# Kernel tuning notes

Measured on AMD Instinct MI355X. Metric: run time of the kernel, lower is better.

Reference implementation:

```python
import jax, jax.numpy as jnp
import numpy as np

K = 3           # spatial kernel size (kernel_size[1]==kernel_size[2])
STRIDE = 1
EPS_BN = 1e-5


def unfold_replicate(t, k=K, stride=STRIDE):
    """t: (b, C, H, W) -> (b, C, k*k, H//stride, W//stride).
    Replicate-padded kxk patches, row-major window order (matches F.pad(replicate)+F.unfold)."""
    b, C, H, W = t.shape
    pad = (k - 1) // 2
    tp = jnp.pad(t, ((0, 0), (0, 0), (pad, pad), (pad, pad)), mode='edge')
    patches = [tp[:, :, di:di + H:stride, dj:dj + W:stride]
               for di in range(k) for dj in range(k)]
    return jnp.stack(patches, axis=2)


def grid_sample_3d(x, grid):
    """Trilinear grid sample, zeros padding, align_corners=True.
    x: (b,c,D,H,W); grid: (b,P,3) normalized (gx,gy,gz) -> (b,c,P)."""
    b, c, D, H, W = x.shape
    ix = (grid[..., 0] + 1.0) * 0.5 * (W - 1)
    iy = (grid[..., 1] + 1.0) * 0.5 * (H - 1)
    iz = (grid[..., 2] + 1.0) * 0.5 * (D - 1)
    x0 = jnp.floor(ix); y0 = jnp.floor(iy); z0 = jnp.floor(iz)
    fx = ix - x0; fy = iy - y0; fz = iz - z0
    x0i = x0.astype(jnp.int32); y0i = y0.astype(jnp.int32); z0i = z0.astype(jnp.int32)
    x_flat = x.reshape(b, c, D * H * W)
    gather = jax.vmap(lambda xf, idx: xf[:, idx])  # (c,N),(P) -> (c,P) per batch
    out = jnp.zeros((b, c, ix.shape[1]), dtype=x.dtype)
    for dz, wz in ((0, 1.0 - fz), (1, fz)):
        zi = z0i + dz
        for dy, wy in ((0, 1.0 - fy), (1, fy)):
            yi = y0i + dy
            for dx, wx in ((0, 1.0 - fx), (1, fx)):
                xi = x0i + dx
                valid = ((zi >= 0) & (zi < D) & (yi >= 0) & (yi < H)
                         & (xi >= 0) & (xi < W))
                idx = (jnp.clip(zi, 0, D - 1) * H + jnp.clip(yi, 0, H - 1)) * W \
                      + jnp.clip(xi, 0, W - 1)
                w = (wz * wy * wx) * valid.astype(x.dtype)
                out = out + w[:, None, :] * gather(x_flat, idx)
    return out


def gca_cost(x, dp, normal, intri):
    b, c, d, H, W = x.shape
    k2 = K * K
    h, w = H // STRIDE, W // STRIDE
    ctr = k2 // 2

    dp_unf = unfold_replicate(dp)        # (b, d, k2, h, w)
    n_unf = unfold_replicate(normal)     # (b, 3, k2, h, w)
    nx, ny, nz = n_unf[:, 0], n_unf[:, 1], n_unf[:, 2]

    fx = intri[:, 0, 0][:, None, None]; fy = intri[:, 1, 1][:, None, None]
    cx = intri[:, 0, 2][:, None, None]; cy = intri[:, 1, 2][:, None, None]
    yg, xg = jnp.meshgrid(jnp.arange(H, dtype=x.dtype),
                          jnp.arange(W, dtype=x.dtype), indexing='ij')
    posx = (xg[None] - cx) / fx          # (b, H, W) normalized camera rays
    posy = (yg[None] - cy) / fy
    pos_unf = unfold_replicate(jnp.stack([posx, posy], axis=1))  # (b,2,k2,h,w)
    pu, pv = pos_unf[:, 0], pos_unf[:, 1]
    pu_c = pu[:, ctr:ctr + 1]; pv_c = pv[:, ctr:ctr + 1]

    num = nx * pu_c + ny * pv_c + nz
    den = nx * pu + ny * pv + nz
    den = jnp.where(jnp.abs(den) < 1e-8, jnp.sign(den) * 1e-8, den)
    wgt = num / den
    wgt = jnp.where(jnp.isfinite(wgt), wgt, 1.0)   # (b, k2, h, w)

    dp_ctr = dp_unf[:, :, ctr]                      # (b, d, h, w)
    dp_prog = wgt[:, None] * dp_ctr[:, :, None]     # (b, d, k2, h, w)
    interval = dp_unf[:, 1] - dp_unf[:, 0]          # (b, k2, h, w)
    z = (dp_prog - dp_unf[:, 0][:, None]) / interval[:, None]  # (b,d,k2,h,w)

    xy = jnp.broadcast_to(jnp.stack([xg, yg], axis=0)[None], (b, 2, H, W))
    xy_unf = unfold_replicate(xy)                   # (b,2,k2,h,w)
    px = jnp.broadcast_to(xy_unf[:, 0][:, None], (b, d, k2, h, w))
    py = jnp.broadcast_to(xy_unf[:, 1][:, None], (b, d, k2, h, w))

    gx = px / ((W - 1) / 2.0) - 1.0
    gy = py / ((H - 1) / 2.0) - 1.0
    gz = z / ((d - 1) / 2.0) - 1.0
    grid = jnp.stack([gx, gy, gz], axis=-1).reshape(b, d * k2 * h * w, 3)

    samp = grid_sample_3d(x, grid)                  # (b, c, d*k2*h*w)
    samp = samp.reshape(b, c, d, k2, h, w).transpose(0, 1, 3, 2, 4, 5)
    return samp.reshape(b, c * k2, d, h, w)


def reference(x, dp, normal, intri, weight, gamma, beta):
    cost = gca_cost(x, dp, normal, intri)
    y = jax.lax.conv_general_dilated(
        cost, weight, window_strides=(1, 1, 1),
        padding=[(1, 1), (0, 0), (0, 0)],
        dimension_numbers=('NCDHW', 'OIDHW', 'NCDHW'))
    # BatchNorm3d (training-mode batch stats, biased var, eps=1e-5) + ReLU
    mean = jnp.mean(y, axis=(0, 2, 3, 4), keepdims=True)
    var = jnp.var(y, axis=(0, 2, 3, 4), keepdims=True)
    g = gamma.reshape(1, -1, 1, 1, 1)
    bta = beta.reshape(1, -1, 1, 1, 1)
    return jax.nn.relu(g * (y - mean) * jax.lax.rsqrt(var + EPS_BN) + bta)


def setup_inputs() -> dict:
    key = jax.random.key(0)
    ks = jax.random.split(key, 6)
    b, c, d, H, W = 1, 8, 32, 128, 128
    out_ch = 16
    x = jax.random.normal(ks[0], (b, c, d, H, W), dtype=jnp.float32)
    # monotone depth hypotheses per pixel (interval = dp[:,1]-dp[:,0] must be nonzero)
    planes = 425.0 + 10.0 * jnp.arange(d, dtype=jnp.float32)
    scale = 1.0 + 0.05 * jax.random.uniform(ks[1], (b, 1, H, W), dtype=jnp.float32)
    dp = planes[None, :, None, None] * scale                    # (b, d, H, W)
    # near-frontal unit normals so plane-homography weights stay well-conditioned
    nxy = 0.2 * jax.random.normal(ks[2], (b, 2, H, W), dtype=jnp.float32)
    nz = 1.0 + 0.1 * jax.random.normal(ks[3], (b, 1, H, W), dtype=jnp.float32)
    n = jnp.concatenate([nxy, nz], axis=1)
    normal = n / jnp.linalg.norm(n, axis=1, keepdims=True)
    intri = jnp.broadcast_to(
        jnp.array([[1100.0, 0.0, W / 2.0],
                   [0.0, 1100.0, H / 2.0],
                   [0.0, 0.0, 1.0]], dtype=jnp.float32), (b, 3, 3))
    weight = 0.05 * jax.random.normal(ks[4], (out_ch, c * K * K, 3, 1, 1),
                                      dtype=jnp.float32)
    gamma = jnp.ones((out_ch,), jnp.float32)
    beta = jnp.zeros((out_ch,), jnp.float32)
    return {"x": x, "dp": dp, "normal": normal, "intri": intri,
            "weight": weight, "gamma": gamma, "beta": beta}
```

## Files before the change

### kernel.cpp

```cpp
#include <hip/hip_runtime.h>
#include <math.h>

#define W_    128
#define H_    128
#define HW    16384
#define D_    32
#define C_IN  8
#define OC    16
#define NRED  524288.0f

#define SXS2  19
#define SXB2  1028
#define SXS   36
#define SXB   1948
#define TILE  2568

typedef __attribute__((ext_vector_type(8))) short bf16x8;
typedef __attribute__((ext_vector_type(4))) float f32x4;

union FragU { uint4 u; bf16x8 h; };


__device__ __forceinline__ unsigned bf16rne(float f) {
    unsigned u = __float_as_uint(f);
    return (u + 0x7fffu + ((u >> 16) & 1u)) >> 16;
}

__device__ __forceinline__ void init_ws(int t, const float* __restrict__ wsrc,
                                        float* __restrict__ ws) {
    if (t < 32) ws[t] = 0.f;
    uint4* af = reinterpret_cast<uint4*>(ws + 64);
    for (int e = t; e < 768; e += 256) {
        int lane = e & 63, pkd = e >> 6;
        int p = pkd / 3, kd = pkd - p * 3;
        int o = lane & 15, kg = lane >> 4;
        int ch = 2 * p + (kg >> 1);
        int jb = (kg & 1) * 8;
        unsigned dw[4];
#pragma unroll
        for (int r2 = 0; r2 < 4; ++r2) {
            int j0 = jb + 2 * r2, j1 = j0 + 1;
            unsigned b0 = (j0 < 9) ? bf16rne(wsrc[(o * 72 + ch * 9 + j0) * 3 + kd]) : 0u;
            unsigned b1 = (j1 < 9) ? bf16rne(wsrc[(o * 72 + ch * 9 + j1) * 3 + kd]) : 0u;
            dw[r2] = b0 | (b1 << 16);
        }
        af[e] = make_uint4(dw[0], dw[1], dw[2], dw[3]);
    }
}

__global__ __launch_bounds__(256) void k_init(const float* __restrict__ wsrc,
                                              float* __restrict__ ws) {
    init_ws((int)threadIdx.x, wsrc, ws);
}

__global__ __launch_bounds__(256) void k_transpose(const float* __restrict__ x,
                                                   unsigned* __restrict__ xtb,
                                                   const float* __restrict__ wsrc,
                                                   float* __restrict__ ws) {
    __shared__ float tile[32 * 132];
    int bid = blockIdx.x;
    int c  = bid >> 7;
    int ry = bid & 127;
    int t  = threadIdx.x;
    if (bid == 0) init_ws(t, wsrc, ws);
    const float* src = x + c * (D_ * HW) + ry * W_;
    for (int k = 0; k < 4; ++k) {
        int e  = t * 4 + k * 1024;
        int z  = e >> 7;
        int rx = e & 127;
        float4 v = *reinterpret_cast<const float4*>(src + z * HW + rx);
        *reinterpret_cast<float4*>(&tile[z * 132 + rx]) = v;
    }
    __syncthreads();
    int rx = t >> 1;
    int zh = (t & 1) * 16;
    unsigned dw[8];
#pragma unroll
    for (int i = 0; i < 8; ++i) {
        float lo = tile[(zh + 2 * i) * 132 + rx];
        float hi = tile[(zh + 2 * i + 1) * 132 + rx];
        asm("v_cvt_pk_bf16_f32 %0, %1, %2" : "=v"(dw[i]) : "v"(lo), "v"(hi));
    }
    unsigned* dst = xtb + (size_t)(c * HW + ry * W_ + rx) * 16 + (t & 1) * 8;
    reinterpret_cast<uint4*>(dst)[0] = make_uint4(dw[0], dw[1], dw[2], dw[3]);
    reinterpret_cast<uint4*>(dst)[1] = make_uint4(dw[4], dw[5], dw[6], dw[7]);
}

__global__ __launch_bounds__(512, 4) void k_main_bf(const unsigned* __restrict__ xtb,
                                                    const float* __restrict__ dp,
                                                    const float* __restrict__ nrm,
                                                    const float* __restrict__ intri,
                                                    const uint4* __restrict__ afr,
                                                    unsigned* __restrict__ ybf,
                                                    float* __restrict__ stats) {
    __shared__ unsigned s_poolU[2 * SXB2];
    __shared__ float s_B[2 * TILE];
    __shared__ float s_wgt[144], s_dp0[144], s_inv[144];
    __shared__ float s_red[64];

    int t   = threadIdx.x;
    int bid = blockIdx.x;
    int r_row = bid >> 3;
    int rx0   = (bid & 7) * 16;

    int seg = t / 144;
    int f   = t - seg * 144;
    int spx = f >> 3;
    int zq  = f & 7;
    int srow = min(max(r_row + seg - 1, 0), H_ - 1);
    int scol = min(max(rx0 - 1 + spx, 0), W_ - 1);
    const unsigned* gsrcU = xtb + (size_t)(srow * W_ + scol) * 16 + zq * 2;
    int colL = seg * 18 + spx;
    int sdst = colL * SXS2 + 1 + 2 * zq;

    uint2 sv;
    if (t < 432) sv = *reinterpret_cast<const uint2*>(gsrcU);

    if (t < 144) {
        int p = t / 9, j = t - p * 9;
        int jd = j / 3;
        int dy = jd - 1, dx = (j - jd * 3) - 1;
        int cpix = rx0 + p;
        int ry  = min(max(r_row + dy, 0), H_ - 1);
        int rxn = min(max(cpix + dx, 0), W_ - 1);
        int nb  = ry * W_ + rxn;
        float fx = intri[0], cx = intri[2], fy = intri[4], cy = intri[5];
        float nx = nrm[nb], ny = nrm[HW + nb], nz = nrm[2 * HW + nb];
        float pu  = ((float)rxn  - cx) / fx;
        float pv  = ((float)ry   - cy) / fy;
        float puc = ((float)cpix - cx) / fx;
        float pvc = ((float)r_row - cy) / fy;
        float num = nx * puc + ny * pvc + nz;
        float den = nx * pu + ny * pv + nz;
        if (fabsf(den) < 1e-8f)
            den = (den > 0.f) ? 1e-8f : ((den < 0.f) ? -1e-8f : 0.f);
        float w = num / den;
        if (!isfinite(w)) w = 1.0f;
        float d0  = dp[nb];
        float itv = dp[HW + nb] - d0;
        s_wgt[t] = w;
        s_dp0[t] = d0;
        s_inv[t] = 1.0f / itv;
    }
    if (t < 324) {
        int b  = t / 162;
        int rm = t - b * 162;
        int col = rm / 3, w3 = rm - col * 3;
        int off = col * SXS2 + ((w3 == 0) ? 0 : (16 + w3));
        s_poolU[b * SXB2 + off] = 0u;
    }
    if (t < 16) s_B[2560 + (t >> 3) * TILE + (t & 7)] = 0.f;
    __syncthreads();
    if (t < 432) {
        s_poolU[sdst]     = sv.x;
        s_poolU[sdst + 1] = sv.y;
    }

    int px = t & 15;
    int d  = t >> 4;
    float dpv = dp[d * HW + r_row * W_ + rx0 + px];

    unsigned idq[9];
    float fza[9];
#pragma unroll
    for (int j = 0; j < 9; ++j) {
        int pj = px * 9 + j;
        int jd = j / 3;
        int jx = j - jd * 3;
        float z   = (s_wgt[pj] * dpv - s_dp0[pj]) * s_inv[pj];
        float zc  = fminf(fmaxf(z, -2.0f), 34.0f);
        float z0f = floorf(zc);
        fza[j] = zc - z0f;
        int s0 = 2 + (int)z0f;
        idq[j] = (unsigned)((jd * 18 + px + jx) * SXS2 + (s0 >> 1))
               | ((unsigned)(s0 & 1) << 16);
    }
    __syncthreads();

    f32x4 acc0 = {0.f, 0.f, 0.f, 0.f};
    f32x4 acc1 = {0.f, 0.f, 0.f, 0.f};
    f32x4 acc2 = {0.f, 0.f, 0.f, 0.f};
    f32x4 acc3 = {0.f, 0.f, 0.f, 0.f};

    int lane = t & 63;
    int wid  = t >> 6;
    int wb   = wid * 4;
    int grp  = lane >> 4;
    unsigned* sBu = reinterpret_cast<unsigned*>(s_B);
    int wrow = (d * 16 + px) * 5;

    for (int c = 0; c < C_IN; ++c) {
        if (c < 7 && t < 432)
            sv = *reinterpret_cast<const uint2*>(gsrcU + (size_t)(c + 1) * (HW * 16));
        const unsigned* PU = s_poolU + (c & 1) * SXB2;
        float cj[9];
#pragma unroll
        for (int j = 0; j < 9; ++j) {
            unsigned v = idq[j];
            unsigned q = v & 0xffffu;
            unsigned p = v >> 16;
            unsigned u0 = PU[q];
            unsigned u1 = PU[q + p];
            float a = __uint_as_float(p ? (u0 & 0xffff0000u) : (u0 << 16));
            float b = __uint_as_float(p ? (u1 << 16) : (u0 & 0xffff0000u));
            cj[j] = fmaf(fza[j], b - a, a);
        }
        unsigned dwv[5];
#pragma unroll
        for (int r2 = 0; r2 < 4; ++r2) {
            asm("v_cvt_pk_bf16_f32 %0, %1, %2"
                : "=v"(dwv[r2]) : "v"(cj[2 * r2]), "v"(cj[2 * r2 + 1]));
        }
        {
            float zz = 0.f;
            asm("v_cvt_pk_bf16_f32 %0, %1, %2"
                : "=v"(dwv[4]) : "v"(cj[8]), "v"(zz));
        }
        {
            int wo = wrow + (c & 1) * TILE;
            sBu[wo + 0] = dwv[0];
            sBu[wo + 1] = dwv[1];
            sBu[wo + 2] = dwv[2];
            sBu[wo + 3] = dwv[3];
            sBu[wo + 4] = dwv[4];
        }
        if (c < 7 && t < 432) {
            int ds2 = ((c + 1) & 1) * SXB2 + sdst;
            s_poolU[ds2]     = sv.x;
            s_poolU[ds2 + 1] = sv.y;
        }
        __syncthreads();

        if (c & 1) {
            int p = c >> 1;
            FragU a0, a1, a2;
            a0.u = afr[(p * 3 + 0) * 64 + lane];
            a1.u = afr[(p * 3 + 1) * 64 + lane];
            a2.u = afr[(p * 3 + 2) * 64 + lane];
            int boff = ((grp & 1) ? 4 : 0) + ((grp >> 1) ? TILE : 0);
#pragma unroll
            for (int q = 0; q < 6; ++q) {
                int db = wb - 1 + q;
                if (db < 0 || db > 31) continue;
                FragU bf;
                int base = (db * 16 + px) * 5 + boff;
                bf.u.x = sBu[base + 0];
                bf.u.y = sBu[base + 1];
                bf.u.z = sBu[base + 2];
                bf.u.w = sBu[base + 3];
                if (q - 0 >= 0 && q - 0 < 4)
                    *(q == 0 ? &acc0 : q == 1 ? &acc1 : q == 2 ? &acc2 : &acc3) =
                        __builtin_amdgcn_mfma_f32_16x16x32_bf16(a0.h, bf.h,
                            *(q == 0 ? &acc0 : q == 1 ? &acc1 : q == 2 ? &acc2 : &acc3), 0, 0, 0);
                if (q - 1 >= 0 && q - 1 < 4)
                    *(q == 1 ? &acc0 : q == 2 ? &acc1 : q == 3 ? &acc2 : &acc3) =
                        __builtin_amdgcn_mfma_f32_16x16x32_bf16(a1.h, bf.h,
                            *(q == 1 ? &acc0 : q == 2 ? &acc1 : q == 3 ? &acc2 : &acc3), 0, 0, 0);
                if (q - 2 >= 0 && q - 2 < 4)
                    *(q == 2 ? &acc0 : q == 3 ? &acc1 : q == 4 ? &acc2 : &acc3) =
                        __builtin_amdgcn_mfma_f32_16x16x32_bf16(a2.h, bf.h,
                            *(q == 2 ? &acc0 : q == 3 ? &acc1 : q == 4 ? &acc2 : &acc3), 0, 0, 0);
            }
            __syncthreads();
        }
    }

    float* s_b = s_B;
    float bns[4], bnq[4];
    int o_l = t >> 7;
    int dd  = (t >> 2) & 31;
    int q4  = t & 3;
#pragma unroll
    for (int oo = 0; oo < 4; ++oo) {
        if (grp == oo) {
#pragma unroll
            for (int r2 = 0; r2 < 4; ++r2) {
                s_b[(r2 * 32 + wb + 0) * 17 + px] = acc0[r2];
                s_b[(r2 * 32 + wb + 1) * 17 + px] = acc1[r2];
                s_b[(r2 * 32 + wb + 2) * 17 + px] = acc2[r2];
                s_b[(r2 * 32 + wb + 3) * 17 + px] = acc3[r2];
            }
        }
        __syncthreads();
        const float* brow = &s_b[(o_l * 32 + dd) * 17 + q4 * 4];
        float4 yv;
        yv.x = brow[0]; yv.y = brow[1]; yv.z = brow[2]; yv.w = brow[3];
        int o = oo * 4 + o_l;
        size_t base = (size_t)(o * 32 + dd) * HW + r_row * W_ + rx0 + q4 * 4;
        unsigned dA, dB;
        asm("v_cvt_pk_bf16_f32 %0, %1, %2" : "=v"(dA) : "v"(yv.x), "v"(yv.y));
        asm("v_cvt_pk_bf16_f32 %0, %1, %2" : "=v"(dB) : "v"(yv.z), "v"(yv.w));
        uint2 wv; wv.x = dA; wv.y = dB;
        reinterpret_cast<uint2*>(ybf)[base >> 2] = wv;
        bns[oo] = yv.x + yv.y + yv.z + yv.w;
        bnq[oo] = yv.x * yv.x + yv.y * yv.y + yv.z * yv.z + yv.w * yv.w;
        __syncthreads();
    }

#pragma unroll
    for (int oo = 0; oo < 4; ++oo) {
        float s = bns[oo], sq = bnq[oo];
#pragma unroll
        for (int m = 1; m < 64; m <<= 1) {
            s  += __shfl_xor(s, m, 64);
            sq += __shfl_xor(sq, m, 64);
        }
        if ((t & 63) == 0) {
            int w = t >> 6;
            s_red[w * 4 + oo]      = s;
            s_red[32 + w * 4 + oo] = sq;
        }
    }
    __syncthreads();
    if (t < 32) {
        int o  = t & 15;
        int oo = o >> 2, wh = o & 3;
        if (t < 16) {
            float s = s_red[(2 * wh) * 4 + oo] + s_red[(2 * wh + 1) * 4 + oo];
            atomicAdd(&stats[o], s);
        } else {
            float sq = s_red[32 + (2 * wh) * 4 + oo] + s_red[32 + (2 * wh + 1) * 4 + oo];
            atomicAdd(&stats[16 + o], sq);
        }
    }
}

__global__ __launch_bounds__(512, 4) void k_main_raw(const float* __restrict__ x,
                                                     const float* __restrict__ dp,
                                                     const float* __restrict__ nrm,
                                                     const float* __restrict__ intri,
                                                     const uint4* __restrict__ afr,
                                                     float* __restrict__ out,
                                                     float* __restrict__ stats) {
    __shared__ float s_pool[2 * SXB];
    __shared__ float s_B[2 * TILE];
    __shared__ float s_wgt[144], s_dp0[144], s_inv[144];
    __shared__ float s_red[64];

    int t   = threadIdx.x;
    int bid = blockIdx.x;
    int r_row = bid >> 3;
    int rx0   = (bid & 7) * 16;

    int seg = t / 144;
    int f   = t - seg * 144;
    int spx = f >> 3;
    int zq  = f & 7;
    int srow = min(max(r_row + seg - 1, 0), H_ - 1);
    int scol = min(max(rx0 - 1 + spx, 0), W_ - 1);
    const float* gsrc_raw = x + (srow * W_ + scol) + (size_t)(zq * 4) * HW;
    int sdst = 4 + (seg * 18 + spx) * SXS + zq * 4;

    float4 sv;
    if (t < 432) {
        sv.x = gsrc_raw[0]; sv.y = gsrc_raw[HW];
        sv.z = gsrc_raw[2 * HW]; sv.w = gsrc_raw[3 * HW];
    }

    if (t < 144) {
        int p = t / 9, j = t - p * 9;
        int jd = j / 3;
        int dy = jd - 1, dx = (j - jd * 3) - 1;
        int cpix = rx0 + p;
        int ry  = min(max(r_row + dy, 0), H_ - 1);
        int rxn = min(max(cpix + dx, 0), W_ - 1);
        int nb  = ry * W_ + rxn;
        float fx = intri[0], cx = intri[2], fy = intri[4], cy = intri[5];
        float nx = nrm[nb], ny = nrm[HW + nb], nz = nrm[2 * HW + nb];
        float pu  = ((float)rxn  - cx) / fx;
        float pv  = ((float)ry   - cy) / fy;
        float puc = ((float)cpix - cx) / fx;
        float pvc = ((float)r_row - cy) / fy;
        float num = nx * puc + ny * pvc + nz;
        float den = nx * pu + ny * pv + nz;
        if (fabsf(den) < 1e-8f)
            den = (den > 0.f) ? 1e-8f : ((den < 0.f) ? -1e-8f : 0.f);
        float w = num / den;
        if (!isfinite(w)) w = 1.0f;
        float d0  = dp[nb];
        float itv = dp[HW + nb] - d0;
        s_wgt[t] = w;
        s_dp0[t] = d0;
        s_inv[t] = 1.0f / itv;
    }
    if (t < 440) {
        int b  = t / 220;
        int rm = t - b * 220;
        int off = (rm < 4) ? rm : (4 + ((rm - 4) >> 2) * SXS + 32 + ((rm - 4) & 3));
        s_pool[b * SXB + off] = 0.f;
    }
    if (t < 16) s_B[2560 + (t >> 3) * TILE + (t & 7)] = 0.f;
    __syncthreads();
    if (t < 432) *reinterpret_cast<float4*>(&s_pool[sdst]) = sv;

    int px = t & 15;
    int d  = t >> 4;
    float dpv = dp[d * HW + r_row * W_ + rx0 + px];

    int   idx[9];
    float fza[9];
#pragma unroll
    for (int j = 0; j < 9; ++j) {
        int pj = px * 9 + j;
        int jd = j / 3;
        int jx = j - jd * 3;
        float z   = (s_wgt[pj] * dpv - s_dp0[pj]) * s_inv[pj];
        float zc  = fminf(fmaxf(z, -2.0f), 34.0f);
        float z0f = floorf(zc);
        fza[j] = zc - z0f;
        idx[j] = (jd * 18 + px + jx) * SXS + (int)z0f;
    }
    __syncthreads();

    f32x4 acc0 = {0.f, 0.f, 0.f, 0.f};
    f32x4 acc1 = {0.f, 0.f, 0.f, 0.f};
    f32x4 acc2 = {0.f, 0.f, 0.f, 0.f};
    f32x4 acc3 = {0.f, 0.f, 0.f, 0.f};

    int lane = t & 63;
    int wid  = t >> 6;
    int wb   = wid * 4;
    int grp  = lane >> 4;
    unsigned* sBu = reinterpret_cast<unsigned*>(s_B);
    int wrow = (d * 16 + px) * 5;

    for (int c = 0; c < C_IN; ++c) {
        if (c < 7 && t < 432) {
            const float* b = gsrc_raw + (size_t)(c + 1) * (D_ * HW);
            sv.x = b[0]; sv.y = b[HW]; sv.z = b[2 * HW]; sv.w = b[3 * HW];
        }
        const float* sxp = &s_pool[(c & 1) * SXB + 4];
        float cj[9];
#pragma unroll
        for (int j = 0; j < 9; ++j) {
            float a = sxp[idx[j]];
            float b = sxp[idx[j] + 1];
            cj[j] = fmaf(fza[j], b - a, a);
        }
        unsigned dwv[5];
#pragma unroll
        for (int r2 = 0; r2 < 4; ++r2) {
            asm("v_cvt_pk_bf16_f32 %0, %1, %2"
                : "=v"(dwv[r2]) : "v"(cj[2 * r2]), "v"(cj[2 * r2 + 1]));
        }
        {
            float zz = 0.f;
            asm("v_cvt_pk_bf16_f32 %0, %1, %2"
                : "=v"(dwv[4]) : "v"(cj[8]), "v"(zz));
        }
        {
            int wo = wrow + (c & 1) * TILE;
            sBu[wo + 0] = dwv[0];
            sBu[wo + 1] = dwv[1];
            sBu[wo + 2] = dwv[2];
            sBu[wo + 3] = dwv[3];
            sBu[wo + 4] = dwv[4];
        }
        if (c < 7 && t < 432) *reinterpret_cast<float4*>(&s_pool[((c + 1) & 1) * SXB + sdst]) = sv;
        __syncthreads();

        if (c & 1) {
            int p = c >> 1;
            FragU a0, a1, a2;
            a0.u = afr[(p * 3 + 0) * 64 + lane];
            a1.u = afr[(p * 3 + 1) * 64 + lane];
            a2.u = afr[(p * 3 + 2) * 64 + lane];
            int boff = ((grp & 1) ? 4 : 0) + ((grp >> 1) ? TILE : 0);
#pragma unroll
            for (int q = 0; q < 6; ++q) {
                int db = wb - 1 + q;
                if (db < 0 || db > 31) continue;
                FragU bf;
                int base = (db * 16 + px) * 5 + boff;
                bf.u.x = sBu[base + 0];
                bf.u.y = sBu[base + 1];
                bf.u.z = sBu[base + 2];
                bf.u.w = sBu[base + 3];
                if (q - 0 >= 0 && q - 0 < 4)
                    *(q == 0 ? &acc0 : q == 1 ? &acc1 : q == 2 ? &acc2 : &acc3) =
                        __builtin_amdgcn_mfma_f32_16x16x32_bf16(a0.h, bf.h,
                            *(q == 0 ? &acc0 : q == 1 ? &acc1 : q == 2 ? &acc2 : &acc3), 0, 0, 0);
                if (q - 1 >= 0 && q - 1 < 4)
                    *(q == 1 ? &acc0 : q == 2 ? &acc1 : q == 3 ? &acc2 : &acc3) =
                        __builtin_amdgcn_mfma_f32_16x16x32_bf16(a1.h, bf.h,
                            *(q == 1 ? &acc0 : q == 2 ? &acc1 : q == 3 ? &acc2 : &acc3), 0, 0, 0);
                if (q - 2 >= 0 && q - 2 < 4)
                    *(q == 2 ? &acc0 : q == 3 ? &acc1 : q == 4 ? &acc2 : &acc3) =
                        __builtin_amdgcn_mfma_f32_16x16x32_bf16(a2.h, bf.h,
                            *(q == 2 ? &acc0 : q == 3 ? &acc1 : q == 4 ? &acc2 : &acc3), 0, 0, 0);
            }
            __syncthreads();
        }
    }

    float* s_b = s_pool;
    float bns[4], bnq[4];
    int o_l = t >> 7;
    int dd  = (t >> 2) & 31;
    int q4  = t & 3;
#pragma unroll
    for (int oo = 0; oo < 4; ++oo) {
        if (grp == oo) {
#pragma unroll
            for (int r2 = 0; r2 < 4; ++r2) {
                s_b[(r2 * 32 + wb + 0) * 17 + px] = acc0[r2];
                s_b[(r2 * 32 + wb + 1) * 17 + px] = acc1[r2];
                s_b[(r2 * 32 + wb + 2) * 17 + px] = acc2[r2];
                s_b[(r2 * 32 + wb + 3) * 17 + px] = acc3[r2];
            }
        }
        __syncthreads();
        const float* brow = &s_b[(o_l * 32 + dd) * 17 + q4 * 4];
        float4 yv;
        yv.x = brow[0]; yv.y = brow[1]; yv.z = brow[2]; yv.w = brow[3];
        int o = oo * 4 + o_l;
        size_t base = (size_t)(o * 32 + dd) * HW + r_row * W_ + rx0 + q4 * 4;
        *reinterpret_cast<float4*>(out + base) = yv;
        bns[oo] = yv.x + yv.y + yv.z + yv.w;
        bnq[oo] = yv.x * yv.x + yv.y * yv.y + yv.z * yv.z + yv.w * yv.w;
        __syncthreads();
    }

#pragma unroll
    for (int oo = 0; oo < 4; ++oo) {
        float s = bns[oo], sq = bnq[oo];
#pragma unroll
        for (int m = 1; m < 64; m <<= 1) {
            s  += __shfl_xor(s, m, 64);
            sq += __shfl_xor(sq, m, 64);
        }
        if ((t & 63) == 0) {
            int w = t >> 6;
            s_red[w * 4 + oo]      = s;
            s_red[32 + w * 4 + oo] = sq;
        }
    }
    __syncthreads();
    if (t < 32) {
        int o  = t & 15;
        int oo = o >> 2, wh = o & 3;
        if (t < 16) {
            float s = s_red[(2 * wh) * 4 + oo] + s_red[(2 * wh + 1) * 4 + oo];
            atomicAdd(&stats[o], s);
        } else {
            float sq = s_red[32 + (2 * wh) * 4 + oo] + s_red[32 + (2 * wh + 1) * 4 + oo];
            atomicAdd(&stats[16 + o], sq);
        }
    }
}

template <bool YBF>
__global__ __launch_bounds__(256) void k_bn(float* __restrict__ out,
                                            const unsigned* __restrict__ ybf,
                                            const float* __restrict__ stats,
                                            const float* __restrict__ gamma,
                                            const float* __restrict__ beta) {
    int i4 = blockIdx.x * 256 + threadIdx.x;
    int o  = i4 >> 17;
    float invN = 1.f / NRED;
    float mean = stats[o] * invN;
    float var  = stats[16 + o] * invN - mean * mean;
    float rstd = rsqrtf(var + 1e-5f);
    float a = gamma[o] * rstd;
    float b = beta[o] - mean * a;
    float4 y;
    if (YBF) {
        uint2 v = reinterpret_cast<const uint2*>(ybf)[i4];
        y.x = __uint_as_float(v.x << 16);
        y.y = __uint_as_float(v.x & 0xffff0000u);
        y.z = __uint_as_float(v.y << 16);
        y.w = __uint_as_float(v.y & 0xffff0000u);
    } else {
        y = reinterpret_cast<float4*>(out)[i4];
    }
    y.x = fmaxf(0.f, fmaf(y.x, a, b));
    y.y = fmaxf(0.f, fmaf(y.y, a, b));
    y.z = fmaxf(0.f, fmaf(y.z, a, b));
    y.w = fmaxf(0.f, fmaf(y.w, a, b));
    reinterpret_cast<float4*>(out)[i4] = y;
}

extern "C" void kernel_launch(void* const* d_in, const int* in_sizes, int n_in,
                              void* d_out, int out_size, void* d_ws, size_t ws_size,
                              hipStream_t stream) {
    const float* x     = (const float*)d_in[0];
    const float* dp    = (const float*)d_in[1];
    const float* nrm   = (const float*)d_in[2];
    const float* intri = (const float*)d_in[3];
    const float* wsrc  = (const float*)d_in[4];
    const float* gamma = (const float*)d_in[5];
    const float* beta  = (const float*)d_in[6];
    float* out = (float*)d_out;
    float* ws  = (float*)d_ws;

    bool ok = ws_size >= (size_t)(8192 + 2097152 + 4194304) * 4;
    unsigned* xtb = (unsigned*)(ws + 8192);
    unsigned* ybf = (unsigned*)(ws + 8192 + 2097152);
    const uint4* afr = (const uint4*)(ws + 64);

    if (ok) {
        hipLaunchKernelGGL(k_transpose, dim3(1024), dim3(256), 0, stream, x, xtb, wsrc, ws);
        hipLaunchKernelGGL(k_main_bf, dim3(1024), dim3(512), 0, stream,
                           xtb, dp, nrm, intri, afr, ybf, ws);
        hipLaunchKernelGGL(k_bn<true>, dim3(8192), dim3(256), 0, stream,
                           out, ybf, ws, gamma, beta);
    } else {
        hipLaunchKernelGGL(k_init, dim3(1), dim3(256), 0, stream, wsrc, ws);
        hipLaunchKernelGGL(k_main_raw, dim3(1024), dim3(512), 0, stream,
                           x, dp, nrm, intri, afr, out, ws);
        hipLaunchKernelGGL(k_bn<false>, dim3(8192), dim3(256), 0, stream,
                           out, ybf, ws, gamma, beta);
    }
}
```

Before: 59.26 us.

## Store depth-pair packed bf16 layout so each trilinear lookup needs one LDS read

The transpose kernel now writes, for each pixel, 37 words, each holding the bf16 pair (z-2, z-1) with zero padding at both ends. The main kernel can then fetch both interpolation endpoints with a single 32-bit LDS load and no parity select, and the explicit zeroing of the pool border goes away. The cost is roughly doubled global storage and traffic for the transposed input (37 words per pixel instead of 16). Staging loads also become five scalar loads per thread instead of one uint2.

```diff
diff --git a/kernel.cpp b/kernel.cpp
--- a/kernel.cpp
+++ b/kernel.cpp
@@ -9,11 +9,11 @@
 #define OC    16
 #define NRED  524288.0f
 
-#define SXS2  19
-#define SXB2  1028
+#define SXS2  37
+#define SXB2  1998
+#define TILE  2568
 #define SXS   36
 #define SXB   1948
-#define TILE  2568
 
 typedef __attribute__((ext_vector_type(8))) short bf16x8;
 typedef __attribute__((ext_vector_type(4))) float f32x4;
@@ -53,11 +53,12 @@
     init_ws((int)threadIdx.x, wsrc, ws);
 }
 
-__global__ __launch_bounds__(256) void k_transpose(const float* __restrict__ x,
-                                                   unsigned* __restrict__ xtb,
-                                                   const float* __restrict__ wsrc,
-                                                   float* __restrict__ ws) {
+__global__ __launch_bounds__(256) void k_transpose_pd(const float* __restrict__ x,
+                                                      unsigned* __restrict__ xpd,
+                                                      const float* __restrict__ wsrc,
+                                                      float* __restrict__ ws) {
     __shared__ float tile[32 * 132];
+    __shared__ unsigned s_D[128 * 37];
     int bid = blockIdx.x;
     int c  = bid >> 7;
     int ry = bid & 127;
@@ -72,21 +73,29 @@
         *reinterpret_cast<float4*>(&tile[z * 132 + rx]) = v;
     }
     __syncthreads();
-    int rx = t >> 1;
-    int zh = (t & 1) * 16;
-    unsigned dw[8];
-#pragma unroll
-    for (int i = 0; i < 8; ++i) {
-        float lo = tile[(zh + 2 * i) * 132 + rx];
-        float hi = tile[(zh + 2 * i + 1) * 132 + rx];
-        asm("v_cvt_pk_bf16_f32 %0, %1, %2" : "=v"(dw[i]) : "v"(lo), "v"(hi));
-    }
-    unsigned* dst = xtb + (size_t)(c * HW + ry * W_ + rx) * 16 + (t & 1) * 8;
-    reinterpret_cast<uint4*>(dst)[0] = make_uint4(dw[0], dw[1], dw[2], dw[3]);
-    reinterpret_cast<uint4*>(dst)[1] = make_uint4(dw[4], dw[5], dw[6], dw[7]);
-}
-
-__global__ __launch_bounds__(512, 4) void k_main_bf(const unsigned* __restrict__ xtb,
+    {
+        int rx = t >> 1;
+        int h  = t & 1;
+        int s0 = h * 19;
+        int ns = 19 - h;
+        for (int i = 0; i < ns; ++i) {
+            int s = s0 + i;
+            int z0 = s - 2, z1 = s - 1;
+            float a = (z0 >= 0 && z0 < 32) ? tile[z0 * 132 + rx] : 0.f;
+            float b = (z1 >= 0 && z1 < 32) ? tile[z1 * 132 + rx] : 0.f;
+            unsigned d;
+            asm("v_cvt_pk_bf16_f32 %0, %1, %2" : "=v"(d) : "v"(a), "v"(b));
+            s_D[rx * 37 + s] = d;
+        }
+    }
+    __syncthreads();
+    unsigned* dst = xpd + (size_t)(c * HW + ry * W_) * 37;
+    const uint4* sd4 = reinterpret_cast<const uint4*>(s_D);
+    uint4* gd4 = reinterpret_cast<uint4*>(dst);
+    for (int i = t; i < 1184; i += 256) gd4[i] = sd4[i];
+}
+
+__global__ __launch_bounds__(512, 4) void k_main_pd(const unsigned* __restrict__ xpd,
                                                     const float* __restrict__ dp,
                                                     const float* __restrict__ nrm,
                                                     const float* __restrict__ intri,
@@ -109,12 +118,18 @@
     int zq  = f & 7;
     int srow = min(max(r_row + seg - 1, 0), H_ - 1);
     int scol = min(max(rx0 - 1 + spx, 0), W_ - 1);
-    const unsigned* gsrcU = xtb + (size_t)(srow * W_ + scol) * 16 + zq * 2;
+    const unsigned* gsrcU = xpd + (size_t)(srow * W_ + scol) * 37;
     int colL = seg * 18 + spx;
-    int sdst = colL * SXS2 + 1 + 2 * zq;
-
-    uint2 sv;
-    if (t < 432) sv = *reinterpret_cast<const uint2*>(gsrcU);
+    int nld  = (zq == 7) ? 2 : 5;
+    int soff = 5 * zq;
+    int sdst = colL * SXS2 + soff;
+
+    unsigned pd[5];
+    if (t < 432) {
+#pragma unroll
+        for (int i = 0; i < 5; ++i)
+            if (i < nld) pd[i] = gsrcU[soff + i];
+    }
 
     if (t < 144) {
         int p = t / 9, j = t - p * 9;
@@ -142,25 +157,19 @@
         s_dp0[t] = d0;
         s_inv[t] = 1.0f / itv;
     }
-    if (t < 324) {
-        int b  = t / 162;
-        int rm = t - b * 162;
-        int col = rm / 3, w3 = rm - col * 3;
-        int off = col * SXS2 + ((w3 == 0) ? 0 : (16 + w3));
-        s_poolU[b * SXB2 + off] = 0u;
-    }
     if (t < 16) s_B[2560 + (t >> 3) * TILE + (t & 7)] = 0.f;
     __syncthreads();
     if (t < 432) {
-        s_poolU[sdst]     = sv.x;
-        s_poolU[sdst + 1] = sv.y;
+#pragma unroll
+        for (int i = 0; i < 5; ++i)
+            if (i < nld) s_poolU[sdst + i] = pd[i];
     }
 
     int px = t & 15;
     int d  = t >> 4;
     float dpv = dp[d * HW + r_row * W_ + rx0 + px];
 
-    unsigned idq[9];
+    int   idq[9];
     float fza[9];
 #pragma unroll
     for (int j = 0; j < 9; ++j) {
@@ -171,9 +180,7 @@
         float zc  = fminf(fmaxf(z, -2.0f), 34.0f);
         float z0f = floorf(zc);
         fza[j] = zc - z0f;
-        int s0 = 2 + (int)z0f;
-        idq[j] = (unsigned)((jd * 18 + px + jx) * SXS2 + (s0 >> 1))
-               | ((unsigned)(s0 & 1) << 16);
+        idq[j] = (jd * 18 + px + jx) * SXS2 + 2 + (int)z0f;
     }
     __syncthreads();
 
@@ -190,19 +197,19 @@
     int wrow = (d * 16 + px) * 5;
 
     for (int c = 0; c < C_IN; ++c) {
-        if (c < 7 && t < 432)
-            sv = *reinterpret_cast<const uint2*>(gsrcU + (size_t)(c + 1) * (HW * 16));
+        if (c < 7 && t < 432) {
+            const unsigned* bp = gsrcU + (size_t)(c + 1) * (HW * 37);
+#pragma unroll
+            for (int i = 0; i < 5; ++i)
+                if (i < nld) pd[i] = bp[soff + i];
+        }
         const unsigned* PU = s_poolU + (c & 1) * SXB2;
         float cj[9];
 #pragma unroll
         for (int j = 0; j < 9; ++j) {
-            unsigned v = idq[j];
-            unsigned q = v & 0xffffu;
-            unsigned p = v >> 16;
-            unsigned u0 = PU[q];
-            unsigned u1 = PU[q + p];
-            float a = __uint_as_float(p ? (u0 & 0xffff0000u) : (u0 << 16));
-            float b = __uint_as_float(p ? (u1 << 16) : (u0 & 0xffff0000u));
+            unsigned u = PU[idq[j]];
+            float a = __uint_as_float(u << 16);
+            float b = __uint_as_float(u & 0xffff0000u);
             cj[j] = fmaf(fza[j], b - a, a);
         }
         unsigned dwv[5];
@@ -226,8 +233,9 @@
         }
         if (c < 7 && t < 432) {
             int ds2 = ((c + 1) & 1) * SXB2 + sdst;
-            s_poolU[ds2]     = sv.x;
-            s_poolU[ds2 + 1] = sv.y;
+#pragma unroll
+            for (int i = 0; i < 5; ++i)
+                if (i < nld) s_poolU[ds2 + i] = pd[i];
         }
         __syncthreads();
 
@@ -593,15 +601,17 @@
     float* out = (float*)d_out;
     float* ws  = (float*)d_ws;
 
-    bool ok = ws_size >= (size_t)(8192 + 2097152 + 4194304) * 4;
-    unsigned* xtb = (unsigned*)(ws + 8192);
-    unsigned* ybf = (unsigned*)(ws + 8192 + 2097152);
+    const size_t XPD = (size_t)37 * HW * C_IN;
+    bool ok = ws_size >= (size_t)(8192 + XPD + 4194304) * 4;
+    unsigned* xpd = (unsigned*)(ws + 8192);
+    unsigned* ybf = (unsigned*)(ws + 8192 + XPD);
     const uint4* afr = (const uint4*)(ws + 64);
 
     if (ok) {
-        hipLaunchKernelGGL(k_transpose, dim3(1024), dim3(256), 0, stream, x, xtb, wsrc, ws);
-        hipLaunchKernelGGL(k_main_bf, dim3(1024), dim3(512), 0, stream,
-                           xtb, dp, nrm, intri, afr, ybf, ws);
+        hipLaunchKernelGGL(k_transpose_pd, dim3(1024), dim3(256), 0, stream,
+                           x, xpd, wsrc, ws);
+        hipLaunchKernelGGL(k_main_pd, dim3(1024), dim3(512), 0, stream,
+                           xpd, dp, nrm, intri, afr, ybf, ws);
         hipLaunchKernelGGL(k_bn<true>, dim3(8192), dim3(256), 0, stream,
                            out, ybf, ws, gamma, beta);
     } else {
```

After: 60.42 us. About the same (+2.0%).
